# Optimization experiments

Hardware: AMD Instinct MI355X
Metric: run time of the kernel (lower is better)

## Reference

```python
import jax, jax.numpy as jnp
import numpy as np

N = 100000        # nodes
E = 1600000       # edges (before self loops)
IN_DIM = 128
OUT_DIM = 64
HEADS = 4
CH = OUT_DIM // HEADS   # 16 channels per head
G = 64            # graphs in batch
EPS = 1e-5        # GraphNorm eps
SLOPE = 0.2       # LeakyReLU negative slope (GATv2Conv default)


def setup_inputs() -> dict:
    key = jax.random.key(0)
    ks = jax.random.split(key, 8)
    x = jax.random.normal(ks[0], (N, IN_DIM), dtype=jnp.float32)
    edge_index = jax.random.randint(ks[1], (2, E), 0, N, dtype=jnp.int64)
    batch = jnp.sort(jax.random.randint(ks[2], (N,), 0, G, dtype=jnp.int64))
    s_in = 1.0 / np.sqrt(IN_DIM)
    # GATv2Conv params (share_weights=False): W_l for source, W_r for target
    Wl = jax.random.normal(ks[3], (IN_DIM, HEADS * CH), dtype=jnp.float32) * s_in
    Wr = jax.random.normal(ks[4], (IN_DIM, HEADS * CH), dtype=jnp.float32) * s_in
    att = jax.random.normal(ks[5], (HEADS, CH), dtype=jnp.float32) * (1.0 / np.sqrt(CH))
    conv_bias = jnp.zeros((HEADS * CH,), dtype=jnp.float32)
    # skip Linear
    skip_W = jax.random.normal(ks[6], (IN_DIM, OUT_DIM), dtype=jnp.float32) * s_in
    skip_b = jax.random.normal(ks[7], (OUT_DIM,), dtype=jnp.float32) * s_in
    # GraphNorm params (PyG init: weight=1, bias=0, mean_scale=1)
    ones = jnp.ones((OUT_DIM,), dtype=jnp.float32)
    zeros = jnp.zeros((OUT_DIM,), dtype=jnp.float32)
    return {
        "x": x, "edge_index": edge_index, "batch": batch,
        "Wl": Wl, "Wr": Wr, "att": att, "conv_bias": conv_bias,
        "skip_W": skip_W, "skip_b": skip_b,
        "bn_w": ones, "bn_b": zeros, "bn_ms": ones,
        "sn_w": ones, "sn_b": zeros, "sn_ms": ones,
    }


def _gatv2(x, Wl, Wr, att, bias, src, dst):
    n = x.shape[0]
    xl = (x @ Wl).reshape(n, HEADS, CH)   # source transform (also the message)
    xr = (x @ Wr).reshape(n, HEADS, CH)   # target transform
    # GATv2: score = a . LeakyReLU(xl[j] + xr[i]) per head
    e = jax.nn.leaky_relu(xl[src] + xr[dst], SLOPE)          # [E,H,C]
    score = jnp.einsum('ehc,hc->eh', e, att)                  # [E,H]
    # segment softmax over edges sharing a target node
    smax = jax.ops.segment_max(score, dst, num_segments=n)    # [N,H]
    ex = jnp.exp(score - smax[dst])
    denom = jax.ops.segment_sum(ex, dst, num_segments=n)
    alpha = ex / denom[dst]                                   # [E,H]
    out = jax.ops.segment_sum(xl[src] * alpha[:, :, None], dst, num_segments=n)
    return out.reshape(n, HEADS * CH) + bias


def _graph_norm(x, w, b, ms, batch):
    cnt = jax.ops.segment_sum(jnp.ones((x.shape[0],), x.dtype), batch, num_segments=G)
    cnt = jnp.maximum(cnt, 1.0)[:, None]
    mean = jax.ops.segment_sum(x, batch, num_segments=G) / cnt
    cen = x - mean[batch] * ms
    var = jax.ops.segment_sum(cen * cen, batch, num_segments=G) / cnt
    inv = jax.lax.rsqrt(var + EPS)
    return w * cen * inv[batch] + b


def reference(x, edge_index, batch, Wl, Wr, att, conv_bias, skip_W, skip_b,
              bn_w, bn_b, bn_ms, sn_w, sn_b, sn_ms):
    n = x.shape[0]
    loop = jnp.arange(n, dtype=edge_index.dtype)  # add_self_loops=True default
    src = jnp.concatenate([edge_index[0], loop])
    dst = jnp.concatenate([edge_index[1], loop])
    x_main = _gatv2(x, Wl, Wr, att, conv_bias, src, dst)
    x_main = _graph_norm(x_main, bn_w, bn_b, bn_ms, batch)
    x_skip = _graph_norm(x @ skip_W + skip_b, sn_w, sn_b, sn_ms, batch)
    return jax.nn.elu(x_main + x_skip)
```

## Files before the change

### kernel.cpp

```cpp
#include <hip/hip_runtime.h>

#define IND 128
#define OUTD 64
#define NG 64
#define NPART 8
#define NSTRIPE 256
#define SLOPE 0.2f
#define EPSV 1e-5f
#define JMASK 131071
#define DEGCAP 48

typedef short bf16x8 __attribute__((ext_vector_type(8)));
typedef float f32x4 __attribute__((ext_vector_type(4)));
typedef float f32x2 __attribute__((ext_vector_type(2)));

__device__ __forceinline__ unsigned bf16rne(float f) {
  unsigned u = __float_as_uint(f);
  return (u + 0x7fffu + ((u >> 16) & 1u)) >> 16;
}
__device__ __forceinline__ unsigned pack2(float a, float b) {
  return bf16rne(a) | (bf16rne(b) << 16);
}

__global__ __launch_bounds__(256) void wcvt_kernel(
    const float* __restrict__ Wl, const float* __restrict__ Wr,
    const float* __restrict__ Ws, unsigned short* __restrict__ wt) {
  int i = blockIdx.x * 256 + threadIdx.x;
  if (i >= 3 * 64 * 128) return;
  int k = i & 127, col = (i >> 7) & 63, which = i >> 13;
  const float* W = (which == 0) ? Wl : (which == 1) ? Wr : Ws;
  int row = which * 64 + col;
  int t = row >> 4, m = row & 15;
  int kc = k >> 5, quad = (k >> 3) & 3, j = k & 7;
  int slot = ((t * 4 + kc) * 4 + quad) * 16 + m;
  wt[slot * 8 + j] = (unsigned short)bf16rne(W[k * OUTD + col]);
}

__device__ __forceinline__ void gemm3_body(
    int bx, const float* __restrict__ x, const unsigned short* __restrict__ wt,
    const float* __restrict__ skip_b,
    unsigned* __restrict__ xlb, float* __restrict__ xr, float* __restrict__ xs,
    int n, unsigned short* wlds) {
  int tid = threadIdx.x;
  int wave = tid >> 6, lane = tid & 63;
  int m = lane & 15, quad = lane >> 4;
  int arow = bx * 64 + wave * 16 + m;
  int arowc = min(arow, n - 1);
  const float* xrow = x + (size_t)arowc * IND;

  f32x4 f0[4], f1[4];
#pragma unroll
  for (int kc = 0; kc < 4; ++kc) {
    int k0 = kc * 32 + quad * 8;
    f0[kc] = __builtin_nontemporal_load((const f32x4*)&xrow[k0]);
    f1[kc] = __builtin_nontemporal_load((const f32x4*)&xrow[k0 + 4]);
  }

#pragma unroll
  for (int i2 = 0; i2 < 12; ++i2) {
    int c = i2 * 256 + tid;
    uint4 v = *(const uint4*)&wt[c * 8];
    *(uint4*)&wlds[c * 8] = v;
  }
  __syncthreads();

  union { uint4 u; bf16x8 v; } af[4];
#pragma unroll
  for (int kc = 0; kc < 4; ++kc)
    af[kc].u = make_uint4(pack2(f0[kc].x, f0[kc].y), pack2(f0[kc].z, f0[kc].w),
                          pack2(f1[kc].x, f1[kc].y), pack2(f1[kc].z, f1[kc].w));

  f32x4 acc[12] = {};
#pragma unroll
  for (int kc = 0; kc < 4; ++kc) {
#pragma unroll
    for (int t = 0; t < 12; ++t) {
      const bf16x8* bp =
          (const bf16x8*)&wlds[(((t * 4 + kc) * 4 + quad) * 16 + m) * 8];
      acc[t] = __builtin_amdgcn_mfma_f32_16x16x32_bf16(af[kc].v, *bp, acc[t], 0, 0, 0);
    }
  }

  float sbv[4];
#pragma unroll
  for (int q = 0; q < 4; ++q) sbv[q] = skip_b[q * 16 + m];

  int orow_base = bx * 64 + wave * 16 + quad * 4;
#pragma unroll
  for (int r = 0; r < 4; ++r) {
    int orow = orow_base + r;
    bool ok = orow < n;
#pragma unroll
    for (int t = 0; t < 4; ++t) {
      float v = acc[t][r];
      float pv = __shfl_xor(v, 1);
      if (ok && !(m & 1))
        xlb[(orow << 5) + t * 8 + (m >> 1)] = pack2(v, pv);
    }
#pragma unroll
    for (int t = 4; t < 8; ++t)
      if (ok) xr[(orow << 6) + (t - 4) * 16 + m] = acc[t][r];
#pragma unroll
    for (int t = 8; t < 12; ++t)
      if (ok) xs[(orow << 6) + (t - 8) * 16 + m] = acc[t][r] + sbv[t - 8];
  }
}

__device__ __forceinline__ void scat1(int d, int s, int lo, int hi,
                                      int* count, int* __restrict__ bucket) {
  if (d >= lo && d < hi) {
    int p = atomicAdd(&count[d], 1);
    if (p < DEGCAP) bucket[d * DEGCAP + p] = s;
  }
}

__device__ __forceinline__ void scatter_body(int r, int stripe,
                                             const int* __restrict__ src,
                                             const int* __restrict__ dst,
                                             int* count, int* __restrict__ bucket,
                                             int E, int n8) {
  int lo = r * n8, hi = lo + n8;
  int per = (((E + NSTRIPE - 1) / NSTRIPE) + 3) & ~3;
  int s0 = stripe * per;
  int s1 = min(E, s0 + per);
  for (int e = s0 + (int)threadIdx.x * 4; e < s1; e += 1024) {
    if (e + 4 <= s1) {
      int4 d4 = *(const int4*)&dst[e];
      int4 s4 = *(const int4*)&src[e];
      scat1(d4.x, s4.x, lo, hi, count, bucket);
      scat1(d4.y, s4.y, lo, hi, count, bucket);
      scat1(d4.z, s4.z, lo, hi, count, bucket);
      scat1(d4.w, s4.w, lo, hi, count, bucket);
    } else {
      for (int q = e; q < s1; ++q)
        scat1(dst[q], src[q], lo, hi, count, bucket);
    }
  }
}

__device__ __forceinline__ void goff_body(int bx, const int* __restrict__ batch,
                                          int* goff, int n) {
  int i = bx * 256 + threadIdx.x;
  if (i >= n) return;
  int b = batch[i];
  int prev = (i == 0) ? -1 : batch[i - 1];
  for (int g = prev + 1; g <= b; ++g) goff[g] = i;
  if (i == n - 1)
    for (int g = b + 1; g <= NG; ++g) goff[g] = n;
}

__global__ __launch_bounds__(256) void mega1_kernel(
    const float* __restrict__ x, const unsigned short* __restrict__ wt,
    const float* __restrict__ skip_b,
    unsigned* __restrict__ xlb, float* __restrict__ xr, float* __restrict__ xs,
    const int* __restrict__ src, const int* __restrict__ dst,
    int* count, int* bucket,
    const int* __restrict__ batch, int* goff,
    int n, int E, int n8, int nbG, int nbB, int SG, int GG) {
  __shared__ unsigned short wlds[3 * 64 * IND];
  int group = blockIdx.x >> 3, pos = blockIdx.x & 7;
  int mn = min(SG, GG), m2 = 2 * mn;
  bool isS;
  int sub;
  if (group < m2) { isS = ((group & 1) == 0); sub = group >> 1; }
  else           { isS = (SG > GG);           sub = mn + (group - m2); }
  if (isS) {
    scatter_body(pos, sub, src, dst, count, bucket, E, n8);
  } else {
    int g = sub * 8 + pos;
    if (g < nbG) gemm3_body(g, x, wt, skip_b, xlb, xr, xs, n, wlds);
    else if (g < nbG + nbB) goff_body(g - nbG, batch, goff, n);
  }
}

__global__ __launch_bounds__(256) void edge_kernel(
    const unsigned* __restrict__ xlb, const float* __restrict__ xr,
    const int* __restrict__ count, const int* __restrict__ bucket,
    const float* __restrict__ att, const float* __restrict__ conv_bias,
    float* __restrict__ out_main, int n) {
  int tid = threadIdx.x;
  int wave = tid >> 6;
  int lane = tid & 63;
  int half = lane >> 5;
  int sub = lane & 31;
  int bx = (int)blockIdx.x;
  int node = bx * 8 + wave * 2 + half;
  bool act = node < n;
  int nodec = min(node, n - 1);
  int base2 = (nodec << 6) | (sub << 1);

  f32x2 xrc = __builtin_nontemporal_load((const f32x2*)&xr[base2]);
  unsigned us = xlb[(nodec << 5) | sub];
  float xs0 = __uint_as_float(us << 16);
  float xs1 = __uint_as_float(us & 0xffff0000u);
  float2 att2 = *(const float2*)&att[sub << 1];

  float t0 = xs0 + xrc.x, t1 = xs1 + xrc.y;
  t0 = fmaxf(t0, SLOPE * t0);
  t1 = fmaxf(t1, SLOPE * t1);
  float s = t0 * att2.x + t1 * att2.y;
  s += __shfl_xor(s, 1);
  s += __shfl_xor(s, 2);
  s += __shfl_xor(s, 4);
  const float sself = s;

  int e0 = nodec * DEGCAP;
  int deg = min(count[nodec], DEGCAP);
  int iters = max(deg, __shfl_xor(deg, 32));

  float denom = 1.f;
  float a0 = xs0, a1 = xs1;
  int i = 0;
  for (; i + 3 < iters; i += 4) {
    float p[4], v0[4], v1[4];
#pragma unroll
    for (int k = 0; k < 4; ++k) {
      bool a = (i + k < deg);
      int e = a ? (e0 + i + k) : e0;
      int j = bucket[e] & JMASK;
      unsigned u = xlb[(j << 5) | sub];
      v0[k] = __uint_as_float(u << 16);
      v1[k] = __uint_as_float(u & 0xffff0000u);
      float tx = v0[k] + xrc.x, ty = v1[k] + xrc.y;
      tx = fmaxf(tx, SLOPE * tx); ty = fmaxf(ty, SLOPE * ty);
      float sc = tx * att2.x + ty * att2.y;
      sc += __shfl_xor(sc, 1);
      sc += __shfl_xor(sc, 2);
      sc += __shfl_xor(sc, 4);
      p[k] = a ? __expf(sc - sself) : 0.f;
    }
#pragma unroll
    for (int k = 0; k < 4; ++k) {
      denom += p[k];
      a0 += p[k] * v0[k];
      a1 += p[k] * v1[k];
    }
  }
  for (; i < iters; ++i) {
    bool a = (i < deg);
    int e = a ? (e0 + i) : e0;
    int j = bucket[e] & JMASK;
    unsigned u = xlb[(j << 5) | sub];
    float v0 = __uint_as_float(u << 16);
    float v1 = __uint_as_float(u & 0xffff0000u);
    float tx = v0 + xrc.x, ty = v1 + xrc.y;
    tx = fmaxf(tx, SLOPE * tx); ty = fmaxf(ty, SLOPE * ty);
    float sc = tx * att2.x + ty * att2.y;
    sc += __shfl_xor(sc, 1);
    sc += __shfl_xor(sc, 2);
    sc += __shfl_xor(sc, 4);
    float p = a ? __expf(sc - sself) : 0.f;
    denom += p;
    a0 += p * v0;
    a1 += p * v1;
  }
  float inv = 1.f / denom;
  float2 cb = *(const float2*)&conv_bias[sub << 1];
  if (act) {
    f32x2 o; o.x = a0 * inv + cb.x; o.y = a1 * inv + cb.y;
    __builtin_nontemporal_store(o, (f32x2*)&out_main[base2]);
  }
}

__global__ __launch_bounds__(256) void stats_part_kernel(
    const float* __restrict__ mainv, const float* __restrict__ xs,
    const int* __restrict__ goff, float* __restrict__ part) {
  int g = blockIdx.x, q = blockIdx.y;
  int start = goff[g], end = goff[g + 1];
  int col = threadIdx.x & 63, grp = threadIdx.x >> 6;
  float s1m = 0.f, s2m = 0.f, s1s = 0.f, s2s = 0.f;
  for (int node = start + q * 4 + grp; node < end; node += 4 * NPART) {
    float vm = __builtin_nontemporal_load(&mainv[(node << 6) | col]);
    float vs = __builtin_nontemporal_load(&xs[(node << 6) | col]);
    s1m += vm; s2m += vm * vm;
    s1s += vs; s2s += vs * vs;
  }
  __shared__ float red[4][4][64];
  red[0][grp][col] = s1m; red[1][grp][col] = s2m;
  red[2][grp][col] = s1s; red[3][grp][col] = s2s;
  __syncthreads();
  if (threadIdx.x < 64) {
    int c = threadIdx.x;
    float* dst = &part[(g * NPART + q) * 256];
#pragma unroll
    for (int st = 0; st < 4; ++st) {
      float s = red[st][0][c] + red[st][1][c] + red[st][2][c] + red[st][3][c];
      dst[st * 64 + c] = s;
    }
  }
}

__global__ void stats_comb_kernel(
    const float* __restrict__ part, const int* __restrict__ goff,
    const float* __restrict__ bn_w, const float* __restrict__ bn_b,
    const float* __restrict__ bn_ms,
    const float* __restrict__ sn_w, const float* __restrict__ sn_b,
    const float* __restrict__ sn_ms,
    float* __restrict__ Am, float* __restrict__ Bm,
    float* __restrict__ As, float* __restrict__ Bs) {
  int g = blockIdx.x;
  int c = threadIdx.x;
  float S1m = 0.f, S2m = 0.f, S1s = 0.f, S2s = 0.f;
  for (int q = 0; q < NPART; ++q) {
    const float* p = &part[(g * NPART + q) * 256];
    S1m += p[c];       S2m += p[64 + c];
    S1s += p[128 + c]; S2s += p[192 + c];
  }
  float cnt = fmaxf((float)(goff[g + 1] - goff[g]), 1.f);
  float meanM = S1m / cnt;
  float aM = meanM * bn_ms[c];
  float varM = S2m / cnt - 2.f * aM * meanM + aM * aM;
  float invM = rsqrtf(varM + EPSV);
  float am = bn_w[c] * invM;
  Am[g * OUTD + c] = am;
  Bm[g * OUTD + c] = bn_b[c] - am * aM;
  float meanS = S1s / cnt;
  float aS = meanS * sn_ms[c];
  float varS = S2s / cnt - 2.f * aS * meanS + aS * aS;
  float invS = rsqrtf(varS + EPSV);
  float as_ = sn_w[c] * invS;
  As[g * OUTD + c] = as_;
  Bs[g * OUTD + c] = sn_b[c] - as_ * aS;
}

__global__ __launch_bounds__(256) void final_kernel(
    const float* __restrict__ xs, const int* __restrict__ batch,
    const float* __restrict__ Am, const float* __restrict__ Bm,
    const float* __restrict__ As, const float* __restrict__ Bs,
    float* out, int n) {
  int idx = blockIdx.x * 256 + threadIdx.x;
  if (idx >= n * 16) return;
  int node = idx >> 4;
  int c4 = (idx & 15) << 2;
  int g = batch[node];
  f32x4 mv = __builtin_nontemporal_load((const f32x4*)&out[idx << 2]);
  f32x4 sv = __builtin_nontemporal_load((const f32x4*)&xs[idx << 2]);
  f32x4 A1 = *(const f32x4*)&Am[g * OUTD + c4];
  f32x4 B1 = *(const f32x4*)&Bm[g * OUTD + c4];
  f32x4 A2 = *(const f32x4*)&As[g * OUTD + c4];
  f32x4 B2 = *(const f32x4*)&Bs[g * OUTD + c4];
  f32x4 v;
  v.x = A1.x * mv.x + B1.x + A2.x * sv.x + B2.x;
  v.y = A1.y * mv.y + B1.y + A2.y * sv.y + B2.y;
  v.z = A1.z * mv.z + B1.z + A2.z * sv.z + B2.z;
  v.w = A1.w * mv.w + B1.w + A2.w * sv.w + B2.w;
  v.x = (v.x > 0.f) ? v.x : (__expf(v.x) - 1.f);
  v.y = (v.y > 0.f) ? v.y : (__expf(v.y) - 1.f);
  v.z = (v.z > 0.f) ? v.z : (__expf(v.z) - 1.f);
  v.w = (v.w > 0.f) ? v.w : (__expf(v.w) - 1.f);
  __builtin_nontemporal_store(v, (f32x4*)&out[idx << 2]);
}

extern "C" void kernel_launch(void* const* d_in, const int* in_sizes, int n_in,
                              void* d_out, int out_size, void* d_ws, size_t ws_size,
                              hipStream_t stream) {
  const float* x        = (const float*)d_in[0];
  const int*   ei       = (const int*)d_in[1];
  const int*   batch    = (const int*)d_in[2];
  const float* Wl       = (const float*)d_in[3];
  const float* Wr       = (const float*)d_in[4];
  const float* att      = (const float*)d_in[5];
  const float* conv_b   = (const float*)d_in[6];
  const float* skip_W   = (const float*)d_in[7];
  const float* skip_b   = (const float*)d_in[8];
  const float* bn_w     = (const float*)d_in[9];
  const float* bn_b     = (const float*)d_in[10];
  const float* bn_ms    = (const float*)d_in[11];
  const float* sn_w     = (const float*)d_in[12];
  const float* sn_b     = (const float*)d_in[13];
  const float* sn_ms    = (const float*)d_in[14];

  int n = in_sizes[0] / IND;
  int E = in_sizes[1] / 2;
  const int* src = ei;
  const int* dst = ei + E;
  float* out = (float*)d_out;

  char* w = (char*)d_ws;
  int* count  = (int*)w;   w += (size_t)(n + 64) * 4;
  int* goff   = (int*)w;   w += (size_t)(NG + 64) * 4;
  float* Am   = (float*)w; w += (size_t)NG * OUTD * 4;
  float* Bm   = (float*)w; w += (size_t)NG * OUTD * 4;
  float* As   = (float*)w; w += (size_t)NG * OUTD * 4;
  float* Bs   = (float*)w; w += (size_t)NG * OUTD * 4;
  float* part = (float*)w; w += (size_t)NG * NPART * 256 * 4;
  unsigned short* wt = (unsigned short*)w; w += (size_t)3 * 64 * IND * 2;
  int* bucket = (int*)w;   w += (size_t)n * DEGCAP * 4;
  unsigned* xlb = (unsigned*)w; w += (size_t)n * 32 * 4;
  float* xr   = (float*)w; w += (size_t)n * OUTD * 4;
  float* xs   = (float*)w; w += (size_t)n * OUTD * 4;

  int n8 = (n + 7) / 8;
  int nbG = (n + 63) / 64;
  int nbB = (n + 255) / 256;
  int SG = NSTRIPE;
  int GG = (nbG + nbB + 7) / 8;

  (void)hipMemsetAsync(count, 0, (size_t)(n + 1) * 4, stream);

  wcvt_kernel<<<(3 * 64 * IND + 255) / 256, 256, 0, stream>>>(Wl, Wr, skip_W, wt);

  mega1_kernel<<<8 * (SG + GG), 256, 0, stream>>>(
      x, wt, skip_b, xlb, xr, xs, src, dst, count, bucket, batch, goff,
      n, E, n8, nbG, nbB, SG, GG);

  edge_kernel<<<(n + 7) / 8, 256, 0, stream>>>(xlb, xr, count, bucket, att, conv_b,
                                               out, n);
  dim3 sg(NG, NPART);
  stats_part_kernel<<<sg, 256, 0, stream>>>(out, xs, goff, part);
  stats_comb_kernel<<<NG, 64, 0, stream>>>(part, goff, bn_w, bn_b, bn_ms,
                                           sn_w, sn_b, sn_ms, Am, Bm, As, Bs);
  final_kernel<<<(n * 16 + 255) / 256, 256, 0, stream>>>(xs, batch, Am, Bm, As, Bs,
                                                         out, n);
}
```

Measured before the change: 340.4 us.

## Stage x tile via direct global-to-LDS loads and read weights from global

After: 326.2 us. 4.2% less time.

```diff
diff --git a/kernel.cpp b/kernel.cpp
--- a/kernel.cpp
+++ b/kernel.cpp
@@ -20,6 +20,15 @@
 }
 __device__ __forceinline__ unsigned pack2(float a, float b) {
   return bf16rne(a) | (bf16rne(b) << 16);
+}
+__device__ __forceinline__ unsigned pack2u(unsigned a, unsigned b) {
+  return pack2(__uint_as_float(a), __uint_as_float(b));
+}
+
+__device__ __forceinline__ void gload_lds16(const void* g, void* l) {
+  __builtin_amdgcn_global_load_lds(
+      (const __attribute__((address_space(1))) void*)g,
+      (__attribute__((address_space(3))) void*)l, 16, 0, 0);
 }
 
 __global__ __launch_bounds__(256) void wcvt_kernel(
@@ -40,35 +49,32 @@
     int bx, const float* __restrict__ x, const unsigned short* __restrict__ wt,
     const float* __restrict__ skip_b,
     unsigned* __restrict__ xlb, float* __restrict__ xr, float* __restrict__ xs,
-    int n, unsigned short* wlds) {
+    int n, uint4* ldsx) {
   int tid = threadIdx.x;
   int wave = tid >> 6, lane = tid & 63;
   int m = lane & 15, quad = lane >> 4;
-  int arow = bx * 64 + wave * 16 + m;
-  int arowc = min(arow, n - 1);
-  const float* xrow = x + (size_t)arowc * IND;
-
-  f32x4 f0[4], f1[4];
+
+#pragma unroll
+  for (int i = 0; i < 8; ++i) {
+    int c = i * 256 + tid;
+    int row = c >> 5, u = c & 31;
+    int us = u ^ (row & 7);
+    int growc = min(bx * 64 + row, n - 1);
+    gload_lds16(x + (size_t)growc * IND + us * 4, &ldsx[c]);
+  }
+  __syncthreads();
+
+  int lbase = (wave * 16 + m) * 32;
+  int swz = m & 7;
+  union { uint4 u; bf16x8 v; } af[4];
 #pragma unroll
   for (int kc = 0; kc < 4; ++kc) {
-    int k0 = kc * 32 + quad * 8;
-    f0[kc] = __builtin_nontemporal_load((const f32x4*)&xrow[k0]);
-    f1[kc] = __builtin_nontemporal_load((const f32x4*)&xrow[k0 + 4]);
-  }
-
-#pragma unroll
-  for (int i2 = 0; i2 < 12; ++i2) {
-    int c = i2 * 256 + tid;
-    uint4 v = *(const uint4*)&wt[c * 8];
-    *(uint4*)&wlds[c * 8] = v;
-  }
-  __syncthreads();
-
-  union { uint4 u; bf16x8 v; } af[4];
-#pragma unroll
-  for (int kc = 0; kc < 4; ++kc)
-    af[kc].u = make_uint4(pack2(f0[kc].x, f0[kc].y), pack2(f0[kc].z, f0[kc].w),
-                          pack2(f1[kc].x, f1[kc].y), pack2(f1[kc].z, f1[kc].w));
+    int u0 = kc * 8 + quad * 2;
+    uint4 A0 = ldsx[lbase + (u0 ^ swz)];
+    uint4 A1 = ldsx[lbase + ((u0 + 1) ^ swz)];
+    af[kc].u = make_uint4(pack2u(A0.x, A0.y), pack2u(A0.z, A0.w),
+                          pack2u(A1.x, A1.y), pack2u(A1.z, A1.w));
+  }
 
   f32x4 acc[12] = {};
 #pragma unroll
@@ -76,7 +82,7 @@
 #pragma unroll
     for (int t = 0; t < 12; ++t) {
       const bf16x8* bp =
-          (const bf16x8*)&wlds[(((t * 4 + kc) * 4 + quad) * 16 + m) * 8];
+          (const bf16x8*)&wt[(((t * 4 + kc) * 4 + quad) * 16 + m) * 8];
       acc[t] = __builtin_amdgcn_mfma_f32_16x16x32_bf16(af[kc].v, *bp, acc[t], 0, 0, 0);
     }
   }
@@ -157,7 +163,7 @@
     int* count, int* bucket,
     const int* __restrict__ batch, int* goff,
     int n, int E, int n8, int nbG, int nbB, int SG, int GG) {
-  __shared__ unsigned short wlds[3 * 64 * IND];
+  __shared__ uint4 ldsx[2048];
   int group = blockIdx.x >> 3, pos = blockIdx.x & 7;
   int mn = min(SG, GG), m2 = 2 * mn;
   bool isS;
@@ -168,7 +174,7 @@
     scatter_body(pos, sub, src, dst, count, bucket, E, n8);
   } else {
     int g = sub * 8 + pos;
-    if (g < nbG) gemm3_body(g, x, wt, skip_b, xlb, xr, xs, n, wlds);
+    if (g < nbG) gemm3_body(g, x, wt, skip_b, xlb, xr, xs, n, ldsx);
     else if (g < nbG + nbB) goff_body(g - nbG, batch, goff, n);
   }
 }
```
